# Kernel tuning notes

Measured on AMD Instinct MI355X. Metric: run time of the kernel, lower is better.

Reference implementation:

```python
import jax, jax.numpy as jnp
import numpy as np

NUM_HEADS = 16
DIM = 1024


def setup_inputs() -> dict:
    key = jax.random.key(0)
    k1, k2, k3, k4 = jax.random.split(key, 4)
    B, N, C = 4, 2048, DIM
    x = jax.random.normal(k1, (B, N, C), dtype=jnp.float32)
    # weights stored in apply orientation: y = x @ W (+ b)
    W_qkv = jax.random.normal(k2, (C, 3 * C), dtype=jnp.float32) * (C ** -0.5)
    W_out = jax.random.normal(k3, (C, C), dtype=jnp.float32) * (C ** -0.5)
    b_out = jax.random.normal(k4, (C,), dtype=jnp.float32) * 0.01
    return {"hidden_states": x, "W_qkv": W_qkv, "W_out": W_out, "b_out": b_out}


def reference(hidden_states, W_qkv, W_out, b_out):
    B, N, C = hidden_states.shape
    H = NUM_HEADS
    Dh = C // H
    scale = Dh ** -0.5
    qkv = hidden_states @ W_qkv                      # [B, N, 3C]
    qkv = qkv.reshape(B, N, 3, H, Dh).transpose(2, 0, 3, 1, 4)  # [3, B, H, N, Dh]
    q, k, v = qkv[0], qkv[1], qkv[2]
    scores = jnp.einsum('bhnd,bhmd->bhnm', q, k) * scale  # [B, H, N, N]
    probs = jax.nn.softmax(scores, axis=-1)
    out = jnp.einsum('bhnm,bhmd->bhnd', probs, v)    # [B, H, N, Dh]
    out = out.transpose(0, 2, 1, 3).reshape(B, N, C)  # merge heads
    return out @ W_out + b_out                        # dropout p=0 -> identity
```

## Files before the change

### kernel.cpp

```cpp
#include <hip/hip_runtime.h>
#include <hip/hip_bf16.h>
#include <stdint.h>

#define BATCH 4
#define SEQN  2048
#define DIMC  1024
#define NHEADS 16
#define DHEAD 64
#define BH_TOT 64
#define MROWS 8192

typedef __attribute__((ext_vector_type(8))) short bf16x8;
typedef __attribute__((ext_vector_type(4))) float f32x4;

__device__ __forceinline__ unsigned short bf16_rtne(float f){
  union { float f; unsigned u; } v; v.f = f;
  unsigned u = v.u;
  return (unsigned short)((u + 0x7FFFu + ((u >> 16) & 1u)) >> 16);
}
__device__ __forceinline__ float bf16f(unsigned short h){
  union { unsigned u; float f; } v; v.u = ((unsigned)h) << 16;
  return v.f;
}
__device__ __forceinline__ unsigned cvt_pk_bf16(float lo, float hi){
  unsigned r;
  asm("v_cvt_pk_bf16_f32 %0, %1, %2" : "=v"(r) : "v"(lo), "v"(hi));
  return r;
}

__device__ __forceinline__ void async16(void* lds, const void* g){
  __builtin_amdgcn_global_load_lds((const __attribute__((address_space(1))) void*)g,
                                   (__attribute__((address_space(3))) void*)lds, 16, 0, 0);
}

__global__ __launch_bounds__(256) void split_rows_k(const float* __restrict__ X,
    unsigned short* __restrict__ O, int nrows, int Kc){
  int q4 = Kc >> 2;
  int total = nrows * q4;
  int idx = blockIdx.x*256 + threadIdx.x;
  if (idx >= total) return;
  int row = idx / q4, c = idx - row*q4;
  const float4 v = *(const float4*)(X + ((size_t)row*Kc + c*4));
  float fv[4] = {v.x, v.y, v.z, v.w};
  unsigned short hi[4], lo[4];
#pragma unroll
  for (int j=0;j<4;j++){ hi[j] = bf16_rtne(fv[j]); lo[j] = bf16_rtne(fv[j] - bf16f(hi[j])); }
  size_t ob = (size_t)row*(2*Kc) + c*4;
  ushort4 h; h.x=hi[0]; h.y=hi[1]; h.z=hi[2]; h.w=hi[3];
  ushort4 l2; l2.x=lo[0]; l2.y=lo[1]; l2.z=lo[2]; l2.w=lo[3];
  *(ushort4*)(O + ob) = h;
  *(ushort4*)(O + ob + Kc) = l2;
}

__global__ __launch_bounds__(256) void transpose_split_k(const float* __restrict__ W,
    unsigned short* __restrict__ Wt, int K, int Nc){
  __shared__ float tile[32][33];
  int tx = threadIdx.x & 31, ty = threadIdx.x >> 5;
  int n0 = blockIdx.x*32, k0 = blockIdx.y*32;
#pragma unroll
  for (int i=0;i<4;i++){
    int k = k0 + ty + i*8;
    tile[ty + i*8][tx] = W[(size_t)k*Nc + n0 + tx];
  }
  __syncthreads();
#pragma unroll
  for (int i=0;i<4;i++){
    int n = n0 + ty + i*8;
    float f = tile[tx][ty + i*8];
    unsigned short hi = bf16_rtne(f);
    unsigned short lo = bf16_rtne(f - bf16f(hi));
    Wt[(size_t)n*(2*K) + k0 + tx] = hi;
    Wt[(size_t)n*(2*K) + K + k0 + tx] = lo;
  }
}

__global__ __launch_bounds__(256) void gemm_split_k(
    const unsigned short* __restrict__ A, const unsigned short* __restrict__ Bt,
    float* __restrict__ C, const float* __restrict__ bias, int M, int Nc, int K)
{
  __shared__ unsigned short a_lds[2][4096];
  __shared__ unsigned short b_lds[2][4096];
  const int t = threadIdx.x, w = t>>6, l = t&63, lg = l>>4, ll = l&15;
  const int wr = w>>1, wc = w&1;
  const int nbx = gridDim.x;
  const int nwg = nbx * gridDim.y;
  const int orig = blockIdx.y*nbx + blockIdx.x;
  const int id = ((orig & 7) * (nwg >> 3)) + (orig >> 3);
  const int m0 = (id % nbx)*128, n0 = (id / nbx)*128;
  const int ldk = 2*K;
  const int nkt = (3*K) >> 5;
  f32x4 acc[4][4];
#pragma unroll
  for (int m=0;m<4;m++)
#pragma unroll
    for (int n=0;n<4;n++) acc[m][n] = (f32x4){0.f,0.f,0.f,0.f};

  auto stage = [&](int buf, int kt){
    int kp = kt*32;
    int ac = (kp < K)   ? kp : kp - K;
    int bc = (kp < 2*K) ? kp : kp - 2*K;
#pragma unroll
    for (int i=0;i<2;i++){
      int s = t + i*256; int row = s>>2; int sl = s&3; int sl2 = sl ^ (row&3);
      async16(&a_lds[buf][s*8], A + (size_t)(m0+row)*ldk + ac + sl2*8);
    }
#pragma unroll
    for (int i=0;i<2;i++){
      int s = t + i*256; int row = s>>2; int sl = s&3; int sl2 = sl ^ (row&3);
      async16(&b_lds[buf][s*8], Bt + (size_t)(n0+row)*ldk + bc + sl2*8);
    }
  };

  stage(0, 0);
  __syncthreads();
  for (int kt=0; kt<nkt; ++kt){
    int cur = kt&1;
    if (kt+1 < nkt) stage(cur^1, kt+1);
    bf16x8 af[4], bfr[4];
#pragma unroll
    for (int m=0;m<4;m++){
      int row = wr*64 + m*16 + ll;
      af[m] = *(const bf16x8*)&a_lds[cur][row*32 + ((lg ^ (row&3))*8)];
    }
#pragma unroll
    for (int n=0;n<4;n++){
      int row = wc*64 + n*16 + ll;
      bfr[n] = *(const bf16x8*)&b_lds[cur][row*32 + ((lg ^ (row&3))*8)];
    }
#pragma unroll
    for (int m=0;m<4;m++)
#pragma unroll
      for (int n=0;n<4;n++)
        acc[m][n] = __builtin_amdgcn_mfma_f32_16x16x32_bf16(af[m], bfr[n], acc[m][n], 0,0,0);
    __syncthreads();
  }
#pragma unroll
  for (int m=0;m<4;m++)
#pragma unroll
    for (int n=0;n<4;n++){
      int col = n0 + wc*64 + n*16 + ll;
      float bv = bias ? bias[col] : 0.f;
#pragma unroll
      for (int r=0;r<4;r++){
        int row = m0 + wr*64 + m*16 + lg*4 + r;
        C[(size_t)row*Nc + col] = acc[m][n][r] + bv;
      }
    }
}

#define QSCALE 0.18033688f
__global__ __launch_bounds__(256) void split_qk_k(const float* __restrict__ qkv,
    unsigned short* __restrict__ Qo, unsigned short* __restrict__ Ko){
  int idx = blockIdx.x*256 + threadIdx.x;
  int d4 = idx & 15, n = (idx>>4) & (SEQN-1), bh = idx >> 15;
  int b = bh>>4, h = bh&15;
  size_t base = ((size_t)(b*SEQN + n))*3072 + h*64 + d4*4;
  float4 q = *(const float4*)(qkv + base);
  float4 k = *(const float4*)(qkv + base + 1024);
  float fq[4] = {q.x*QSCALE, q.y*QSCALE, q.z*QSCALE, q.w*QSCALE};
  float fk[4] = {k.x, k.y, k.z, k.w};
  unsigned short qh[4], ql[4], kh[4];
#pragma unroll
  for (int j=0;j<4;j++){
    qh[j] = bf16_rtne(fq[j]); ql[j] = bf16_rtne(fq[j] - bf16f(qh[j]));
    kh[j] = bf16_rtne(fk[j]);
  }
  size_t obq = ((size_t)bh*SEQN + n)*128 + d4*4;
  size_t obk = ((size_t)bh*SEQN + n)*64 + d4*4;
  ushort4 u;
  u.x=qh[0];u.y=qh[1];u.z=qh[2];u.w=qh[3]; *(ushort4*)(Qo+obq) = u;
  u.x=ql[0];u.y=ql[1];u.z=ql[2];u.w=ql[3]; *(ushort4*)(Qo+obq+64) = u;
  u.x=kh[0];u.y=kh[1];u.z=kh[2];u.w=kh[3]; *(ushort4*)(Ko+obk) = u;
}

__global__ __launch_bounds__(256) void build_vt_k(const float* __restrict__ qkv,
    unsigned short* __restrict__ Vt){
  __shared__ float tile[64][65];
  const int mt = blockIdx.x, bh = blockIdx.y;
  const int b = bh>>4, h = bh&15;
  const int t = threadIdx.x;
  const int r = t>>2, seg = t&3;
  size_t src = ((size_t)(b*SEQN + mt*64 + r))*3072 + 2048 + h*64 + seg*16;
#pragma unroll
  for (int j=0;j<4;j++){
    float4 v = *(const float4*)(qkv + src + j*4);
    tile[r][seg*16 + j*4 + 0] = v.x;
    tile[r][seg*16 + j*4 + 1] = v.y;
    tile[r][seg*16 + j*4 + 2] = v.z;
    tile[r][seg*16 + j*4 + 3] = v.w;
  }
  __syncthreads();
  const int d = r, ms = seg;
  unsigned short o16[16];
#pragma unroll
  for (int j=0;j<16;j++) o16[j] = bf16_rtne(tile[ms*16 + j][d]);
  size_t dst = ((size_t)(bh*64 + d))*SEQN + mt*64 + ms*16;
  uint4 u0, u1;
  unsigned* pu = (unsigned*)&u0;
  unsigned* pv = (unsigned*)&u1;
#pragma unroll
  for (int j=0;j<4;j++){
    pu[j] = (unsigned)o16[2*j]   | ((unsigned)o16[2*j+1]<<16);
    pv[j] = (unsigned)o16[8+2*j] | ((unsigned)o16[9+2*j]<<16);
  }
  *(uint4*)(Vt + dst) = u0;
  *(uint4*)(Vt + dst + 8) = u1;
}

__global__ __launch_bounds__(256, 4) void attn_k(const unsigned short* __restrict__ Q,
    const unsigned short* __restrict__ Kh, const unsigned short* __restrict__ Vt,
    float* __restrict__ att)
{
  __shared__ unsigned short k_lds[2][4096];
  __shared__ unsigned short v_lds[2][4096];
  __shared__ unsigned p_lds[4][512];
  const int orig = blockIdx.y*gridDim.x + blockIdx.x;
  const int id = ((orig & 7) << 8) + (orig >> 3);
  const int qt = id & 31, bh = id >> 5;
  const int b = bh>>4, h = bh&15;
  const int t = threadIdx.x, w = t>>6, l = t&63, lg = l>>4, ll = l&15;
  const size_t kvbase = (size_t)bh*SEQN;

  bf16x8 qf[4];
  {
    size_t qrow = (kvbase + qt*64 + w*16 + ll) * 128;
#pragma unroll
    for (int i=0;i<4;i++)
      qf[i] = *(const bf16x8*)(Q + qrow + i*32 + lg*8);
  }
  f32x4 o[4];
#pragma unroll
  for (int d=0; d<4; d++) o[d] = (f32x4){0.f,0.f,0.f,0.f};
  float lsum = 0.f;

  auto stage = [&](int buf, int kv){
    int m0 = kv*64;
#pragma unroll
    for (int i=0;i<2;i++){
      int s = t + i*256; int row = s>>3; int sl = s&7; int sl2 = sl ^ (row&7);
      async16(&k_lds[buf][s*8], Kh + (kvbase + m0 + row)*64 + sl2*8);
    }
#pragma unroll
    for (int i=0;i<2;i++){
      int s = t + i*256; int row = s>>3; int sl = s&7; int sl2 = sl ^ (row&7);
      async16(&v_lds[buf][s*8], Vt + ((size_t)bh*64 + row)*SEQN + m0 + sl2*8);
    }
  };

  stage(0, 0);
  __syncthreads();
  const int NKV = SEQN/64;
  for (int kv=0; kv<NKV; ++kv){
    int cur = kv&1;
    if (kv+1 < NKV) stage(cur^1, kv+1);
#pragma unroll
    for (int nt=0; nt<4; ++nt){
      int row = nt*16 + ll;
      bf16x8 kf0 = *(const bf16x8*)&k_lds[cur][row*64 + (((0*4+lg) ^ (row&7))*8)];
      bf16x8 kf1 = *(const bf16x8*)&k_lds[cur][row*64 + (((1*4+lg) ^ (row&7))*8)];
      f32x4 a = (f32x4){0.f,0.f,0.f,0.f};
      __builtin_amdgcn_s_setprio(1);
      a = __builtin_amdgcn_mfma_f32_16x16x32_bf16(kf0, qf[0], a, 0,0,0);
      a = __builtin_amdgcn_mfma_f32_16x16x32_bf16(kf1, qf[1], a, 0,0,0);
      a = __builtin_amdgcn_mfma_f32_16x16x32_bf16(kf0, qf[2], a, 0,0,0);
      a = __builtin_amdgcn_mfma_f32_16x16x32_bf16(kf1, qf[3], a, 0,0,0);
      __builtin_amdgcn_s_setprio(0);
      float e0 = exp2f(a[0]), e1 = exp2f(a[1]), e2 = exp2f(a[2]), e3 = exp2f(a[3]);
      lsum += (e0 + e1) + (e2 + e3);
      unsigned pk0 = cvt_pk_bf16(e0, e1);
      unsigned pk1 = cvt_pk_bf16(e2, e3);
      int c0 = nt*8 + lg*2;
      int addr = ll*32 + (((c0>>2) ^ (ll&7))<<2) + (c0&3);
      *(uint2*)&p_lds[w][addr] = make_uint2(pk0, pk1);
    }
#pragma unroll
    for (int ks=0; ks<2; ++ks){
      int chunk = ks*4 + lg;
      bf16x8 pf = *(const bf16x8*)&p_lds[w][ll*32 + ((chunk ^ (ll&7))<<2)];
      __builtin_amdgcn_s_setprio(1);
#pragma unroll
      for (int dt=0; dt<4; ++dt){
        int row = dt*16 + ll;
        bf16x8 vf = *(const bf16x8*)&v_lds[cur][row*64 + (((ks*4+lg) ^ (row&7))*8)];
        o[dt] = __builtin_amdgcn_mfma_f32_16x16x32_bf16(pf, vf, o[dt], 0,0,0);
      }
      __builtin_amdgcn_s_setprio(0);
    }
    __syncthreads();
  }
  float tot = lsum;
  tot += __shfl_xor(tot, 16);
  tot += __shfl_xor(tot, 32);
  float inv = 1.0f / tot;
#pragma unroll
  for (int r=0;r<4;r++){
    float rl = __shfl(inv, lg*4 + r);
    int qrow = qt*64 + w*16 + lg*4 + r;
    size_t ob = ((size_t)(b*SEQN + qrow))*DIMC + h*64;
#pragma unroll
    for (int dt=0; dt<4; ++dt)
      att[ob + dt*16 + ll] = o[dt][r] * rl;
  }
}

extern "C" void kernel_launch(void* const* d_in, const int* in_sizes, int n_in,
                              void* d_out, int out_size, void* d_ws, size_t ws_size,
                              hipStream_t stream){
  const float* x    = (const float*)d_in[0];
  const float* Wqkv = (const float*)d_in[1];
  const float* Wout = (const float*)d_in[2];
  const float* bout = (const float*)d_in[3];
  float* out = (float*)d_out;

  char* ws = (char*)d_ws;
  size_t off = 0;
  auto walloc = [&](size_t bytes) -> void* {
    void* p = ws + off; off += (bytes + 255) & ~(size_t)255; return p;
  };
  unsigned short* x_hl   = (unsigned short*)walloc((size_t)MROWS*2048*2);
  unsigned short* wqkv_t = (unsigned short*)walloc((size_t)3072*2048*2);
  float*          qkv    = (float*)walloc((size_t)MROWS*3072*4);
  unsigned short* q_hl   = (unsigned short*)walloc((size_t)BH_TOT*SEQN*128*2);
  unsigned short* k_h    = (unsigned short*)walloc((size_t)BH_TOT*SEQN*64*2);
  unsigned short* vt     = (unsigned short*)walloc((size_t)BH_TOT*64*SEQN*2);
  unsigned short* wout_t = (unsigned short*)walloc((size_t)1024*2048*2);
  float*          att    = qkv;
  unsigned short* att_hl = x_hl;

  split_rows_k<<<8192, 256, 0, stream>>>(x, x_hl, MROWS, DIMC);
  transpose_split_k<<<dim3(3072/32, 1024/32), 256, 0, stream>>>(Wqkv, wqkv_t, 1024, 3072);
  transpose_split_k<<<dim3(1024/32, 1024/32), 256, 0, stream>>>(Wout, wout_t, 1024, 1024);
  gemm_split_k<<<dim3(MROWS/128, 3072/128), 256, 0, stream>>>(x_hl, wqkv_t, qkv, nullptr, MROWS, 3072, 1024);
  split_qk_k<<<(BH_TOT*SEQN*16)/256, 256, 0, stream>>>(qkv, q_hl, k_h);
  build_vt_k<<<dim3(SEQN/64, BH_TOT), 256, 0, stream>>>(qkv, vt);
  attn_k<<<dim3(SEQN/64, BH_TOT), 256, 0, stream>>>(q_hl, k_h, vt, att);
  split_rows_k<<<8192, 256, 0, stream>>>(att, att_hl, MROWS, DIMC);
  gemm_split_k<<<dim3(MROWS/128, 1024/128), 256, 0, stream>>>(att_hl, wout_t, out, bout, MROWS, 1024, 1024);
}
```

Before: 545.8 us.

## Drop activation lo split, double query tile in attention, emit bf16 attention output

Activations are now rounded to a single bf16 instead of a hi/lo pair, so the GEMMs run two K passes instead of three (A·Bhi and A·Blo). The attention kernel handles 128 query rows per block with two subtiles that share each K/V LDS tile, and writes bf16 output directly, which removes the separate split pass before the output projection. The GEMM LDS layout changes to a fragment-major order without swizzle. Together these cut MFMA work, launches and memory traffic, at the cost of accuracy from dropping the activation low part and more registers in attention.

```diff
diff --git a/kernel.cpp b/kernel.cpp
--- a/kernel.cpp
+++ b/kernel.cpp
@@ -33,23 +33,22 @@
                                    (__attribute__((address_space(3))) void*)lds, 16, 0, 0);
 }
 
-__global__ __launch_bounds__(256) void split_rows_k(const float* __restrict__ X,
+__global__ __launch_bounds__(256) void round_rows_k(const float* __restrict__ X,
     unsigned short* __restrict__ O, int nrows, int Kc){
-  int q4 = Kc >> 2;
-  int total = nrows * q4;
+  int q8 = Kc >> 3;
+  int total = nrows * q8;
   int idx = blockIdx.x*256 + threadIdx.x;
   if (idx >= total) return;
-  int row = idx / q4, c = idx - row*q4;
-  const float4 v = *(const float4*)(X + ((size_t)row*Kc + c*4));
-  float fv[4] = {v.x, v.y, v.z, v.w};
-  unsigned short hi[4], lo[4];
-#pragma unroll
-  for (int j=0;j<4;j++){ hi[j] = bf16_rtne(fv[j]); lo[j] = bf16_rtne(fv[j] - bf16f(hi[j])); }
-  size_t ob = (size_t)row*(2*Kc) + c*4;
-  ushort4 h; h.x=hi[0]; h.y=hi[1]; h.z=hi[2]; h.w=hi[3];
-  ushort4 l2; l2.x=lo[0]; l2.y=lo[1]; l2.z=lo[2]; l2.w=lo[3];
-  *(ushort4*)(O + ob) = h;
-  *(ushort4*)(O + ob + Kc) = l2;
+  size_t base = (size_t)idx * 8;
+  const float4 v0 = *(const float4*)(X + base);
+  const float4 v1 = *(const float4*)(X + base + 4);
+  float fv[8] = {v0.x,v0.y,v0.z,v0.w,v1.x,v1.y,v1.z,v1.w};
+  uint4 u;
+  unsigned* pu = (unsigned*)&u;
+#pragma unroll
+  for (int j=0;j<4;j++)
+    pu[j] = (unsigned)bf16_rtne(fv[2*j]) | ((unsigned)bf16_rtne(fv[2*j+1])<<16);
+  *(uint4*)(O + base) = u;
 }
 
 __global__ __launch_bounds__(256) void transpose_split_k(const float* __restrict__ W,
@@ -74,7 +73,7 @@
   }
 }
 
-__global__ __launch_bounds__(256) void gemm_split_k(
+__global__ __launch_bounds__(256) void gemm_h_k(
     const unsigned short* __restrict__ A, const unsigned short* __restrict__ Bt,
     float* __restrict__ C, const float* __restrict__ bias, int M, int Nc, int K)
 {
@@ -88,7 +87,7 @@
   const int id = ((orig & 7) * (nwg >> 3)) + (orig >> 3);
   const int m0 = (id % nbx)*128, n0 = (id / nbx)*128;
   const int ldk = 2*K;
-  const int nkt = (3*K) >> 5;
+  const int nkt = (2*K) >> 5;
   f32x4 acc[4][4];
 #pragma unroll
   for (int m=0;m<4;m++)
@@ -97,17 +96,19 @@
 
   auto stage = [&](int buf, int kt){
     int kp = kt*32;
-    int ac = (kp < K)   ? kp : kp - K;
-    int bc = (kp < 2*K) ? kp : kp - 2*K;
+    int ac = (kp < K) ? kp : kp - K;
+    int bc = kp;
 #pragma unroll
     for (int i=0;i<2;i++){
-      int s = t + i*256; int row = s>>2; int sl = s&3; int sl2 = sl ^ (row&3);
-      async16(&a_lds[buf][s*8], A + (size_t)(m0+row)*ldk + ac + sl2*8);
+      int s = i*256 + t;
+      async16(&a_lds[buf][s*8],
+              A + (size_t)(m0 + (s>>6)*16 + (s&15))*K + ac + ((s>>4)&3)*8);
     }
 #pragma unroll
     for (int i=0;i<2;i++){
-      int s = t + i*256; int row = s>>2; int sl = s&3; int sl2 = sl ^ (row&3);
-      async16(&b_lds[buf][s*8], Bt + (size_t)(n0+row)*ldk + bc + sl2*8);
+      int s = i*256 + t;
+      async16(&b_lds[buf][s*8],
+              Bt + (size_t)(n0 + (s>>6)*16 + (s&15))*ldk + bc + ((s>>4)&3)*8);
     }
   };
 
@@ -118,15 +119,11 @@
     if (kt+1 < nkt) stage(cur^1, kt+1);
     bf16x8 af[4], bfr[4];
 #pragma unroll
-    for (int m=0;m<4;m++){
-      int row = wr*64 + m*16 + ll;
-      af[m] = *(const bf16x8*)&a_lds[cur][row*32 + ((lg ^ (row&3))*8)];
-    }
-#pragma unroll
-    for (int n=0;n<4;n++){
-      int row = wc*64 + n*16 + ll;
-      bfr[n] = *(const bf16x8*)&b_lds[cur][row*32 + ((lg ^ (row&3))*8)];
-    }
+    for (int m=0;m<4;m++)
+      af[m] = *(const bf16x8*)&a_lds[cur][(wr*4+m)*512 + l*8];
+#pragma unroll
+    for (int n=0;n<4;n++)
+      bfr[n] = *(const bf16x8*)&b_lds[cur][(wc*4+n)*512 + l*8];
 #pragma unroll
     for (int m=0;m<4;m++)
 #pragma unroll
@@ -207,31 +204,34 @@
   *(uint4*)(Vt + dst + 8) = u1;
 }
 
-__global__ __launch_bounds__(256, 4) void attn_k(const unsigned short* __restrict__ Q,
+__global__ __launch_bounds__(256) void attn_k(const unsigned short* __restrict__ Q,
     const unsigned short* __restrict__ Kh, const unsigned short* __restrict__ Vt,
-    float* __restrict__ att)
+    unsigned short* __restrict__ att_h)
 {
   __shared__ unsigned short k_lds[2][4096];
   __shared__ unsigned short v_lds[2][4096];
-  __shared__ unsigned p_lds[4][512];
+  __shared__ unsigned p_lds[4][2][512];
   const int orig = blockIdx.y*gridDim.x + blockIdx.x;
-  const int id = ((orig & 7) << 8) + (orig >> 3);
-  const int qt = id & 31, bh = id >> 5;
+  const int id = ((orig & 7) << 7) + (orig >> 3);
+  const int qt = id & 15, bh = id >> 4;
   const int b = bh>>4, h = bh&15;
   const int t = threadIdx.x, w = t>>6, l = t&63, lg = l>>4, ll = l&15;
   const size_t kvbase = (size_t)bh*SEQN;
 
-  bf16x8 qf[4];
-  {
-    size_t qrow = (kvbase + qt*64 + w*16 + ll) * 128;
+  bf16x8 qf[2][4];
+#pragma unroll
+  for (int sub=0; sub<2; ++sub){
+    size_t qrow = (kvbase + qt*128 + sub*64 + w*16 + ll) * 128;
 #pragma unroll
     for (int i=0;i<4;i++)
-      qf[i] = *(const bf16x8*)(Q + qrow + i*32 + lg*8);
-  }
-  f32x4 o[4];
-#pragma unroll
-  for (int d=0; d<4; d++) o[d] = (f32x4){0.f,0.f,0.f,0.f};
-  float lsum = 0.f;
+      qf[sub][i] = *(const bf16x8*)(Q + qrow + i*32 + lg*8);
+  }
+  f32x4 o[2][4];
+#pragma unroll
+  for (int sub=0; sub<2; ++sub)
+#pragma unroll
+    for (int d=0; d<4; d++) o[sub][d] = (f32x4){0.f,0.f,0.f,0.f};
+  float lsum[2] = {0.f, 0.f};
 
   auto stage = [&](int buf, int kv){
     int m0 = kv*64;
@@ -258,48 +258,63 @@
       int row = nt*16 + ll;
       bf16x8 kf0 = *(const bf16x8*)&k_lds[cur][row*64 + (((0*4+lg) ^ (row&7))*8)];
       bf16x8 kf1 = *(const bf16x8*)&k_lds[cur][row*64 + (((1*4+lg) ^ (row&7))*8)];
-      f32x4 a = (f32x4){0.f,0.f,0.f,0.f};
+      f32x4 a0 = (f32x4){0.f,0.f,0.f,0.f};
+      f32x4 a1 = (f32x4){0.f,0.f,0.f,0.f};
       __builtin_amdgcn_s_setprio(1);
-      a = __builtin_amdgcn_mfma_f32_16x16x32_bf16(kf0, qf[0], a, 0,0,0);
-      a = __builtin_amdgcn_mfma_f32_16x16x32_bf16(kf1, qf[1], a, 0,0,0);
-      a = __builtin_amdgcn_mfma_f32_16x16x32_bf16(kf0, qf[2], a, 0,0,0);
-      a = __builtin_amdgcn_mfma_f32_16x16x32_bf16(kf1, qf[3], a, 0,0,0);
+      a0 = __builtin_amdgcn_mfma_f32_16x16x32_bf16(kf0, qf[0][0], a0, 0,0,0);
+      a0 = __builtin_amdgcn_mfma_f32_16x16x32_bf16(kf1, qf[0][1], a0, 0,0,0);
+      a0 = __builtin_amdgcn_mfma_f32_16x16x32_bf16(kf0, qf[0][2], a0, 0,0,0);
+      a0 = __builtin_amdgcn_mfma_f32_16x16x32_bf16(kf1, qf[0][3], a0, 0,0,0);
+      a1 = __builtin_amdgcn_mfma_f32_16x16x32_bf16(kf0, qf[1][0], a1, 0,0,0);
+      a1 = __builtin_amdgcn_mfma_f32_16x16x32_bf16(kf1, qf[1][1], a1, 0,0,0);
+      a1 = __builtin_amdgcn_mfma_f32_16x16x32_bf16(kf0, qf[1][2], a1, 0,0,0);
+      a1 = __builtin_amdgcn_mfma_f32_16x16x32_bf16(kf1, qf[1][3], a1, 0,0,0);
       __builtin_amdgcn_s_setprio(0);
-      float e0 = exp2f(a[0]), e1 = exp2f(a[1]), e2 = exp2f(a[2]), e3 = exp2f(a[3]);
-      lsum += (e0 + e1) + (e2 + e3);
-      unsigned pk0 = cvt_pk_bf16(e0, e1);
-      unsigned pk1 = cvt_pk_bf16(e2, e3);
       int c0 = nt*8 + lg*2;
       int addr = ll*32 + (((c0>>2) ^ (ll&7))<<2) + (c0&3);
-      *(uint2*)&p_lds[w][addr] = make_uint2(pk0, pk1);
+      {
+        float e0 = exp2f(a0[0]), e1 = exp2f(a0[1]), e2 = exp2f(a0[2]), e3 = exp2f(a0[3]);
+        lsum[0] += (e0 + e1) + (e2 + e3);
+        *(uint2*)&p_lds[w][0][addr] = make_uint2(cvt_pk_bf16(e0,e1), cvt_pk_bf16(e2,e3));
+      }
+      {
+        float e0 = exp2f(a1[0]), e1 = exp2f(a1[1]), e2 = exp2f(a1[2]), e3 = exp2f(a1[3]);
+        lsum[1] += (e0 + e1) + (e2 + e3);
+        *(uint2*)&p_lds[w][1][addr] = make_uint2(cvt_pk_bf16(e0,e1), cvt_pk_bf16(e2,e3));
+      }
     }
 #pragma unroll
     for (int ks=0; ks<2; ++ks){
       int chunk = ks*4 + lg;
-      bf16x8 pf = *(const bf16x8*)&p_lds[w][ll*32 + ((chunk ^ (ll&7))<<2)];
+      bf16x8 pf0 = *(const bf16x8*)&p_lds[w][0][ll*32 + ((chunk ^ (ll&7))<<2)];
+      bf16x8 pf1 = *(const bf16x8*)&p_lds[w][1][ll*32 + ((chunk ^ (ll&7))<<2)];
       __builtin_amdgcn_s_setprio(1);
 #pragma unroll
       for (int dt=0; dt<4; ++dt){
         int row = dt*16 + ll;
         bf16x8 vf = *(const bf16x8*)&v_lds[cur][row*64 + (((ks*4+lg) ^ (row&7))*8)];
-        o[dt] = __builtin_amdgcn_mfma_f32_16x16x32_bf16(pf, vf, o[dt], 0,0,0);
+        o[0][dt] = __builtin_amdgcn_mfma_f32_16x16x32_bf16(pf0, vf, o[0][dt], 0,0,0);
+        o[1][dt] = __builtin_amdgcn_mfma_f32_16x16x32_bf16(pf1, vf, o[1][dt], 0,0,0);
       }
       __builtin_amdgcn_s_setprio(0);
     }
     __syncthreads();
   }
-  float tot = lsum;
-  tot += __shfl_xor(tot, 16);
-  tot += __shfl_xor(tot, 32);
-  float inv = 1.0f / tot;
-#pragma unroll
-  for (int r=0;r<4;r++){
-    float rl = __shfl(inv, lg*4 + r);
-    int qrow = qt*64 + w*16 + lg*4 + r;
-    size_t ob = ((size_t)(b*SEQN + qrow))*DIMC + h*64;
-#pragma unroll
-    for (int dt=0; dt<4; ++dt)
-      att[ob + dt*16 + ll] = o[dt][r] * rl;
+#pragma unroll
+  for (int sub=0; sub<2; ++sub){
+    float tot = lsum[sub];
+    tot += __shfl_xor(tot, 16);
+    tot += __shfl_xor(tot, 32);
+    float inv = 1.0f / tot;
+#pragma unroll
+    for (int r=0;r<4;r++){
+      float rl = __shfl(inv, lg*4 + r);
+      int qrow = qt*128 + sub*64 + w*16 + lg*4 + r;
+      size_t ob = ((size_t)(b*SEQN + qrow))*DIMC + h*64;
+#pragma unroll
+      for (int dt=0; dt<4; ++dt)
+        att_h[ob + dt*16 + ll] = bf16_rtne(o[sub][dt][r] * rl);
+    }
   }
 }
 
@@ -317,23 +332,21 @@
   auto walloc = [&](size_t bytes) -> void* {
     void* p = ws + off; off += (bytes + 255) & ~(size_t)255; return p;
   };
-  unsigned short* x_hl   = (unsigned short*)walloc((size_t)MROWS*2048*2);
+  unsigned short* x_h    = (unsigned short*)walloc((size_t)MROWS*1024*2);
   unsigned short* wqkv_t = (unsigned short*)walloc((size_t)3072*2048*2);
   float*          qkv    = (float*)walloc((size_t)MROWS*3072*4);
   unsigned short* q_hl   = (unsigned short*)walloc((size_t)BH_TOT*SEQN*128*2);
   unsigned short* k_h    = (unsigned short*)walloc((size_t)BH_TOT*SEQN*64*2);
   unsigned short* vt     = (unsigned short*)walloc((size_t)BH_TOT*64*SEQN*2);
   unsigned short* wout_t = (unsigned short*)walloc((size_t)1024*2048*2);
-  float*          att    = qkv;
-  unsigned short* att_hl = x_hl;
-
-  split_rows_k<<<8192, 256, 0, stream>>>(x, x_hl, MROWS, DIMC);
+  unsigned short* att_h  = x_h;
+
+  round_rows_k<<<4096, 256, 0, stream>>>(x, x_h, MROWS, DIMC);
   transpose_split_k<<<dim3(3072/32, 1024/32), 256, 0, stream>>>(Wqkv, wqkv_t, 1024, 3072);
   transpose_split_k<<<dim3(1024/32, 1024/32), 256, 0, stream>>>(Wout, wout_t, 1024, 1024);
-  gemm_split_k<<<dim3(MROWS/128, 3072/128), 256, 0, stream>>>(x_hl, wqkv_t, qkv, nullptr, MROWS, 3072, 1024);
+  gemm_h_k<<<dim3(64, 24), 256, 0, stream>>>(x_h, wqkv_t, qkv, nullptr, MROWS, 3072, 1024);
   split_qk_k<<<(BH_TOT*SEQN*16)/256, 256, 0, stream>>>(qkv, q_hl, k_h);
   build_vt_k<<<dim3(SEQN/64, BH_TOT), 256, 0, stream>>>(qkv, vt);
-  attn_k<<<dim3(SEQN/64, BH_TOT), 256, 0, stream>>>(q_hl, k_h, vt, att);
-  split_rows_k<<<8192, 256, 0, stream>>>(att, att_hl, MROWS, DIMC);
-  gemm_split_k<<<dim3(MROWS/128, 1024/128), 256, 0, stream>>>(att_hl, wout_t, out, bout, MROWS, 1024, 1024);
-}
+  attn_k<<<dim3(16, BH_TOT), 256, 0, stream>>>(q_hl, k_h, vt, att_h);
+  gemm_h_k<<<dim3(64, 8), 256, 0, stream>>>(att_h, wout_t, out, bout, MROWS, 1024, 1024);
+}
```

Result: faster. 524.5 us (-3.9%).
